# Kernel optimization log

Hardware: AMD Instinct MI355X
Metric: run time of the kernel (lower is better)

Reference implementation:

```python
import jax, jax.numpy as jnp
import numpy as np

N_HEADS = 8
D_K = 64
SCALE = D_K ** -0.5


def setup_inputs() -> dict:
    key = jax.random.key(0)
    ks = jax.random.split(key, 5)
    B, C, H, W = 4, 512, 32, 32
    x = jax.random.normal(ks[0], (B, C, H, W), dtype=jnp.float32)
    Wp = jax.random.normal(ks[1], (3 * N_HEADS * D_K, C), dtype=jnp.float32) * (C ** -0.5)
    bp = jax.random.normal(ks[2], (3 * N_HEADS * D_K,), dtype=jnp.float32) * 0.02
    Wo = jax.random.normal(ks[3], (C, N_HEADS * D_K), dtype=jnp.float32) * ((N_HEADS * D_K) ** -0.5)
    bo = jax.random.normal(ks[4], (C,), dtype=jnp.float32) * 0.02
    return {"x": x, "Wp": Wp, "bp": bp, "Wo": Wo, "bo": bo}


def reference(x, Wp, bp, Wo, bo):
    # x: [B, C, H, W]; NOTE: the torch module defines GroupNorm but never calls it.
    B, C, H, W = x.shape
    s = H * W
    xs = x.reshape(B, C, s).transpose(0, 2, 1)          # [B, s, C]
    qkv = (xs @ Wp.T + bp).reshape(B, s, N_HEADS, 3 * D_K)
    q, k, v = jnp.split(qkv, 3, axis=-1)                 # each [B, s, h, d]
    attn = jnp.einsum('bihd,bjhd->bijh', q, k) * SCALE   # [B, s, s, h]
    attn = jax.nn.softmax(attn, axis=2)                  # softmax over j (keys)
    res = jnp.einsum('bijh,bjhd->bihd', attn, v)         # [B, s, h, d]
    res = res.reshape(B, s, N_HEADS * D_K)
    out = res @ Wo.T + bo + xs                           # residual add
    return out.transpose(0, 2, 1).reshape(B, C, H, W)
```

## Files before the change

kernel.cpp:

```cpp
#include <hip/hip_runtime.h>
#include <hip/hip_bf16.h>

typedef unsigned short u16;
typedef __attribute__((ext_vector_type(8))) short frag_ab;
typedef __attribute__((ext_vector_type(4))) float f32x4;
typedef _Float16 f16;
typedef __attribute__((ext_vector_type(4))) _Float16 f16x4;

#define LOG2E 1.44269504088896f

__device__ __forceinline__ float fast_exp2(float x) {
    return __builtin_amdgcn_exp2f(x);
}

__device__ __forceinline__ void gload_lds16(const u16* g, u16* s) {
    __builtin_amdgcn_global_load_lds((const __attribute__((address_space(1))) void*)g,
                                     (__attribute__((address_space(3))) void*)s, 16, 0, 0);
}

__device__ __forceinline__ void gemm64x128_bt_mainloop(
    const u16* __restrict__ A, const u16* __restrict__ B, int K,
    int m0, int n0, f32x4 acc[2][4], u16* As, u16* Bs)
{
    const int tid = threadIdx.x;
    const int lane = tid & 63, quad = lane >> 4, l16 = lane & 15;
    const int wr = ((tid >> 7) & 1) * 32;
    const int wc = ((tid >> 6) & 1) * 64;
    const int srow = tid >> 3;
    const int scol = (tid & 7) * 8;

    for (int k0 = 0; k0 < K; k0 += 64) {
        __syncthreads();
        #pragma unroll
        for (int p = 0; p < 2; ++p) {
            const int r = srow + p * 32;
            gload_lds16(A + (size_t)(m0 + r) * K + k0 + scol, As + r * 64 + scol);
        }
        #pragma unroll
        for (int p = 0; p < 4; ++p) {
            const int r = srow + p * 32;
            gload_lds16(B + (size_t)(n0 + r) * K + k0 + scol, Bs + r * 64 + scol);
        }
        __syncthreads();
        #pragma unroll
        for (int ks = 0; ks < 2; ++ks) {
            frag_ab a[2], b[4];
            #pragma unroll
            for (int mt = 0; mt < 2; ++mt)
                a[mt] = *(const frag_ab*)(As + (wr + mt * 16 + l16) * 64 + ks * 32 + quad * 8);
            #pragma unroll
            for (int nt = 0; nt < 4; ++nt)
                b[nt] = *(const frag_ab*)(Bs + (wc + nt * 16 + l16) * 64 + ks * 32 + quad * 8);
            #pragma unroll
            for (int mt = 0; mt < 2; ++mt)
                #pragma unroll
                for (int nt = 0; nt < 4; ++nt)
                    acc[mt][nt] = __builtin_amdgcn_mfma_f32_16x16x32_bf16(a[mt], b[nt], acc[mt][nt], 0, 0, 0);
        }
    }
}

__device__ __forceinline__ void gemm64x64_bt_mainloop(
    const u16* __restrict__ A, const u16* __restrict__ B, int K,
    int m0, int n0, f32x4 acc[2][2], u16* As, u16* Bs)
{
    const int tid = threadIdx.x;
    const int lane = tid & 63, quad = lane >> 4, l16 = lane & 15;
    const int wr = ((tid >> 7) & 1) * 32;
    const int wc = ((tid >> 6) & 1) * 32;
    const int srow = tid >> 3;
    const int scol = (tid & 7) * 8;

    for (int k0 = 0; k0 < K; k0 += 64) {
        __syncthreads();
        #pragma unroll
        for (int p = 0; p < 2; ++p) {
            const int r = srow + p * 32;
            gload_lds16(A + (size_t)(m0 + r) * K + k0 + scol, As + r * 64 + scol);
            gload_lds16(B + (size_t)(n0 + r) * K + k0 + scol, Bs + r * 64 + scol);
        }
        __syncthreads();
        #pragma unroll
        for (int ks = 0; ks < 2; ++ks) {
            frag_ab a[2], b[2];
            #pragma unroll
            for (int mt = 0; mt < 2; ++mt)
                a[mt] = *(const frag_ab*)(As + (wr + mt * 16 + l16) * 64 + ks * 32 + quad * 8);
            #pragma unroll
            for (int nt = 0; nt < 2; ++nt)
                b[nt] = *(const frag_ab*)(Bs + (wc + nt * 16 + l16) * 64 + ks * 32 + quad * 8);
            #pragma unroll
            for (int mt = 0; mt < 2; ++mt)
                #pragma unroll
                for (int nt = 0; nt < 2; ++nt)
                    acc[mt][nt] = __builtin_amdgcn_mfma_f32_16x16x32_bf16(a[mt], b[nt], acc[mt][nt], 0, 0, 0);
        }
    }
}

__global__ __launch_bounds__(256) void prep_kernel(
    const float* __restrict__ x, __hip_bfloat16* __restrict__ xs_bf,
    const float* __restrict__ Wp, const float* __restrict__ Wo,
    __hip_bfloat16* __restrict__ w_bf)
{
    __shared__ float tile[32][33];
    const int tid = threadIdx.x;
    const int id = blockIdx.x;
    if (id < 2048) {
        const int i0 = (id & 31) * 32;
        const int c0 = ((id >> 5) & 15) * 32;
        const int b  = id >> 9;
        const int tx = tid & 31, ty = tid >> 5;
        const float* xp = x + ((size_t)b * 512 + c0) * 1024 + i0;
        #pragma unroll
        for (int r = ty; r < 32; r += 8)
            tile[r][tx] = xp[(size_t)r * 1024 + tx];
        __syncthreads();
        __hip_bfloat16* op = xs_bf + ((size_t)b * 1024 + i0) * 512 + c0;
        #pragma unroll
        for (int r = ty; r < 32; r += 8)
            op[(size_t)r * 512 + tx] = __float2bfloat16(tile[tx][r]);
    } else {
        const int t = (id - 2048) * 256 + tid;
        const int i4 = t * 4;
        const float* src = (i4 < 786432) ? (Wp + i4) : (Wo + (i4 - 786432));
        const float4 v = *(const float4*)src;
        ushort4 o;
        o.x = __bfloat16_as_ushort(__float2bfloat16(v.x));
        o.y = __bfloat16_as_ushort(__float2bfloat16(v.y));
        o.z = __bfloat16_as_ushort(__float2bfloat16(v.z));
        o.w = __bfloat16_as_ushort(__float2bfloat16(v.w));
        *(ushort4*)((u16*)w_bf + i4) = o;
    }
}

__global__ __launch_bounds__(256) void qkv_gemm_kernel(
    const u16* __restrict__ Wpb, const u16* __restrict__ xsb,
    const float* __restrict__ bp,
    u16* __restrict__ Qb, u16* __restrict__ Kb, f16* __restrict__ VtT)
{
    __shared__ u16 lds[12288];
    u16* As = lds;
    u16* Bs = lds + 4096;
    f32x4 acc[2][4];
    #pragma unroll
    for (int mt = 0; mt < 2; ++mt)
        #pragma unroll
        for (int nt = 0; nt < 4; ++nt)
            { acc[mt][nt][0]=0.f; acc[mt][nt][1]=0.f; acc[mt][nt][2]=0.f; acc[mt][nt][3]=0.f; }
    const int m0 = blockIdx.y * 64;
    const int n0 = blockIdx.x * 128;
    gemm64x128_bt_mainloop(Wpb, xsb, 512, m0, n0, acc, As, Bs);

    const int tid = threadIdx.x;
    const int lane = tid & 63, quad = lane >> 4, l16 = lane & 15;
    const int wr = ((tid >> 7) & 1) * 32, wc = ((tid >> 6) & 1) * 64;
    const int h = blockIdx.y / 3, part = blockIdx.y % 3;
    const int b = blockIdx.x >> 3, ipb = (blockIdx.x & 7) * 128;
    const size_t bh = (size_t)(b * 8 + h);

    if (part < 2) {
        const float scale = (part == 0) ? (0.125f * LOG2E) : 1.0f;
        __syncthreads();
        u16* T = lds;
        #pragma unroll
        for (int nt = 0; nt < 4; ++nt) {
            const int px = wc + nt * 16 + l16;
            #pragma unroll
            for (int mt = 0; mt < 2; ++mt) {
                const int cb = m0 + wr + mt * 16 + quad * 4;
                ushort4 pk;
                pk.x = __bfloat16_as_ushort(__float2bfloat16((acc[mt][nt][0] + bp[cb + 0]) * scale));
                pk.y = __bfloat16_as_ushort(__float2bfloat16((acc[mt][nt][1] + bp[cb + 1]) * scale));
                pk.z = __bfloat16_as_ushort(__float2bfloat16((acc[mt][nt][2] + bp[cb + 2]) * scale));
                pk.w = __bfloat16_as_ushort(__float2bfloat16((acc[mt][nt][3] + bp[cb + 3]) * scale));
                *(ushort4*)&T[px * 72 + wr + mt * 16 + quad * 4] = pk;
            }
        }
        __syncthreads();
        u16* dst = (part == 0 ? Qb : Kb);
        #pragma unroll
        for (int p = 0; p < 4; ++p) {
            const int row = p * 32 + (tid >> 3);
            const int ch8 = (tid & 7) * 8;
            uint4 rv = *(uint4*)&T[row * 72 + ch8];
            *(uint4*)(dst + ((bh * 1024 + ipb + row) << 6) + ch8) = rv;
        }
    } else {
        f16* dst = VtT + bh * 65536;
        #pragma unroll
        for (int mt = 0; mt < 2; ++mt) {
            #pragma unroll
            for (int r = 0; r < 4; ++r) {
                const int d = wr + mt * 16 + quad * 4 + r;
                const float bias = bp[m0 + d];
                #pragma unroll
                for (int nt = 0; nt < 4; ++nt) {
                    const int j = ipb + wc + nt * 16 + l16;
                    dst[(size_t)(j >> 3) * 512 + d * 8 + (j & 7)] =
                        (f16)(acc[mt][nt][r] + bias);
                }
            }
        }
    }
}

__global__ __launch_bounds__(256, 2) void attn_kernel(
    const u16* __restrict__ Qb, const u16* __restrict__ Kb,
    const f16* __restrict__ VtT, __hip_bfloat16* __restrict__ resb)
{
    __shared__ float Opart[4][32][68];
    __shared__ float Lpart[4][4][16];
    const int bh = blockIdx.x;
    const int it = blockIdx.y;
    const int tid = threadIdx.x;
    const int w = tid >> 6, lane = tid & 63, quad = lane >> 4, l16 = lane & 15;

    const u16* Qp = Qb + (size_t)bh * 65536;
    const u16* Kp = Kb + (size_t)bh * 65536;
    const f16* Vp = VtT + (size_t)bh * 65536;

    frag_ab bq[4][2];
    #pragma unroll
    for (int ig = 0; ig < 4; ++ig) {
        const u16* qptr = Qp + (size_t)(it * 64 + ig * 16 + l16) * 64 + quad * 8;
        bq[ig][0] = *(const frag_ab*)(qptr);
        bq[ig][1] = *(const frag_ab*)(qptr + 32);
    }

    f32x4 o[4][4];
    #pragma unroll
    for (int ig = 0; ig < 4; ++ig)
        #pragma unroll
        for (int dt = 0; dt < 4; ++dt)
            { o[ig][dt][0]=0.f; o[ig][dt][1]=0.f; o[ig][dt][2]=0.f; o[ig][dt][3]=0.f; }
    float l_acc[4] = {0.f, 0.f, 0.f, 0.f};

    const u16* kbase = Kp + (size_t)(w * 32 + l16) * 64 + quad * 8;
    const f16* vbase = Vp + (size_t)(w * 4 + (quad >> 1)) * 512 + l16 * 8 + (quad & 1) * 4;

#define LOADKV(JT, KA, VA) do {                                              \
        const u16* kp_ = kbase + (size_t)(JT) * 8192;                        \
        KA[0][0] = *(const frag_ab*)(kp_);                                   \
        KA[0][1] = *(const frag_ab*)(kp_ + 32);                              \
        KA[1][0] = *(const frag_ab*)(kp_ + 1024);                            \
        KA[1][1] = *(const frag_ab*)(kp_ + 1056);                            \
        const f16* vp_ = vbase + (size_t)(JT) * 8192;                        \
        _Pragma("unroll")                                                    \
        for (int dt_ = 0; dt_ < 4; ++dt_) {                                  \
            VA[dt_][0] = *(const f16x4*)(vp_ + dt_ * 128);                   \
            VA[dt_][1] = *(const f16x4*)(vp_ + 1024 + dt_ * 128);            \
        }                                                                    \
    } while (0)

#define COMPUTE(KA, VA) do {                                                 \
        _Pragma("unroll")                                                    \
        for (int ig = 0; ig < 4; ++ig) {                                     \
            f32x4 st0 = {0.f, 0.f, 0.f, 0.f}, st1 = {0.f, 0.f, 0.f, 0.f};    \
            st0 = __builtin_amdgcn_mfma_f32_16x16x32_bf16(KA[0][0], bq[ig][0], st0, 0, 0, 0); \
            st0 = __builtin_amdgcn_mfma_f32_16x16x32_bf16(KA[0][1], bq[ig][1], st0, 0, 0, 0); \
            st1 = __builtin_amdgcn_mfma_f32_16x16x32_bf16(KA[1][0], bq[ig][0], st1, 0, 0, 0); \
            st1 = __builtin_amdgcn_mfma_f32_16x16x32_bf16(KA[1][1], bq[ig][1], st1, 0, 0, 0); \
            f16x4 p0, p1;                                                    \
            float s = 0.f;                                                   \
            _Pragma("unroll")                                                \
            for (int r = 0; r < 4; ++r) {                                    \
                const float e0 = fast_exp2(st0[r]);                          \
                const float e1 = fast_exp2(st1[r]);                          \
                s += e0 + e1;                                                \
                p0[r] = (f16)e0;                                             \
                p1[r] = (f16)e1;                                             \
            }                                                                \
            l_acc[ig] += s;                                                  \
            _Pragma("unroll")                                                \
            for (int dt = 0; dt < 4; ++dt) {                                 \
                o[ig][dt] = __builtin_amdgcn_mfma_f32_16x16x16f16(VA[dt][0], p0, o[ig][dt], 0, 0, 0); \
                o[ig][dt] = __builtin_amdgcn_mfma_f32_16x16x16f16(VA[dt][1], p1, o[ig][dt], 0, 0, 0); \
            }                                                                \
        }                                                                    \
    } while (0)

    frag_ab ka0[2][2], ka1[2][2];
    f16x4 va0[4][2], va1[4][2];
    LOADKV(0, ka0, va0);
    #pragma unroll
    for (int jt = 0; jt < 8; jt += 2) {
        LOADKV(jt + 1, ka1, va1);
        COMPUTE(ka0, va0);
        if (jt < 6)
            LOADKV(jt + 2, ka0, va0);
        COMPUTE(ka1, va1);
    }
#undef LOADKV
#undef COMPUTE

    #pragma unroll
    for (int ig = 0; ig < 4; ++ig) {
        l_acc[ig] += __shfl_xor(l_acc[ig], 16);
        l_acc[ig] += __shfl_xor(l_acc[ig], 32);
    }
    if (lane < 16) {
        #pragma unroll
        for (int ig = 0; ig < 4; ++ig)
            Lpart[w][ig][lane] = l_acc[ig];
    }

    const int bb = bh >> 3, hh = bh & 7;
    const int il = tid >> 3, d0 = (tid & 7) * 8;
    #pragma unroll
    for (int ph = 0; ph < 2; ++ph) {
        __syncthreads();
        #pragma unroll
        for (int g = 0; g < 2; ++g) {
            const int ig = ph * 2 + g;
            #pragma unroll
            for (int dt = 0; dt < 4; ++dt)
                *(f32x4*)&Opart[w][g * 16 + l16][dt * 16 + quad * 4] = o[ig][dt];
        }
        __syncthreads();
        f32x4 sa = *(const f32x4*)&Opart[0][il][d0];
        f32x4 sb = *(const f32x4*)&Opart[0][il][d0 + 4];
        #pragma unroll
        for (int ww = 1; ww < 4; ++ww) {
            sa += *(const f32x4*)&Opart[ww][il][d0];
            sb += *(const f32x4*)&Opart[ww][il][d0 + 4];
        }
        const int ig = ph * 2 + (il >> 4);
        const float linv = 1.f / (Lpart[0][ig][il & 15] + Lpart[1][ig][il & 15] +
                                  Lpart[2][ig][il & 15] + Lpart[3][ig][il & 15]);
        u16 pk[8];
        #pragma unroll
        for (int e = 0; e < 4; ++e) {
            pk[e]     = __bfloat16_as_ushort(__float2bfloat16(sa[e] * linv));
            pk[e + 4] = __bfloat16_as_ushort(__float2bfloat16(sb[e] * linv));
        }
        u16* orow = (u16*)resb +
            ((size_t)(bb * 1024 + it * 64 + ph * 32 + il)) * 512 + hh * 64 + d0;
        *(uint4*)orow = *(uint4*)pk;
    }
}

__global__ __launch_bounds__(256) void out_gemm_kernel(
    const u16* __restrict__ Wob, const u16* __restrict__ resb,
    const float* __restrict__ bo, const float* __restrict__ x,
    float* __restrict__ out)
{
    __shared__ u16 As[64 * 64];
    __shared__ u16 Bs[64 * 64];
    f32x4 acc[2][2];
    #pragma unroll
    for (int mt = 0; mt < 2; ++mt)
        #pragma unroll
        for (int nt = 0; nt < 2; ++nt)
            { acc[mt][nt][0]=0.f; acc[mt][nt][1]=0.f; acc[mt][nt][2]=0.f; acc[mt][nt][3]=0.f; }
    const int m0 = blockIdx.x * 64;
    const int n0 = blockIdx.y * 64;
    gemm64x64_bt_mainloop(Wob, resb, 512, m0, n0, acc, As, Bs);

    const int tid = threadIdx.x;
    const int lane = tid & 63, quad = lane >> 4, l16 = lane & 15;
    const int wr = ((tid >> 7) & 1) * 32, wc = ((tid >> 6) & 1) * 32;
    #pragma unroll
    for (int nt = 0; nt < 2; ++nt) {
        const int pix = n0 + wc + nt * 16 + l16;
        const int b = pix >> 10, ip = pix & 1023;
        #pragma unroll
        for (int mt = 0; mt < 2; ++mt) {
            #pragma unroll
            for (int r = 0; r < 4; ++r) {
                const int c = m0 + wr + mt * 16 + quad * 4 + r;
                const size_t oidx = (((size_t)b * 512 + c) << 10) + ip;
                out[oidx] = acc[mt][nt][r] + bo[c] + x[oidx];
            }
        }
    }
}

extern "C" void kernel_launch(void* const* d_in, const int* in_sizes, int n_in,
                              void* d_out, int out_size, void* d_ws, size_t ws_size,
                              hipStream_t stream)
{
    const float* x  = (const float*)d_in[0];
    const float* Wp = (const float*)d_in[1];
    const float* bp = (const float*)d_in[2];
    const float* Wo = (const float*)d_in[3];
    const float* bo = (const float*)d_in[4];
    float* out = (float*)d_out;

    char* ws = (char*)d_ws;
    size_t off = 0;
    auto carve = [&](size_t bytes) -> void* {
        void* ptr = ws + off;
        off += (bytes + 255) & ~(size_t)255;
        return ptr;
    };
    __hip_bfloat16* xs_bf = (__hip_bfloat16*)carve((size_t)4096 * 512 * 2);
    __hip_bfloat16* Wp_bf = (__hip_bfloat16*)carve((size_t)1536 * 512 * 2);
    __hip_bfloat16* Wo_bf = (__hip_bfloat16*)carve((size_t)512 * 512 * 2);
    u16*            Qb    = (u16*)carve((size_t)32 * 1024 * 64 * 2);
    u16*            Kb    = (u16*)carve((size_t)32 * 1024 * 64 * 2);
    f16*            VtT   = (f16*)carve((size_t)32 * 1024 * 64 * 2);
    __hip_bfloat16* resb  = (__hip_bfloat16*)carve((size_t)4096 * 512 * 2);

    prep_kernel<<<dim3(3072), 256, 0, stream>>>(x, xs_bf, Wp, Wo, Wp_bf);
    qkv_gemm_kernel<<<dim3(32, 24), 256, 0, stream>>>(
        (const u16*)Wp_bf, (const u16*)xs_bf, bp, Qb, Kb, VtT);
    attn_kernel<<<dim3(32, 16), 256, 0, stream>>>(Qb, Kb, VtT, resb);
    out_gemm_kernel<<<dim3(8, 64), 256, 0, stream>>>(
        (const u16*)Wo_bf, (const u16*)resb, bo, x, out);
    (void)Wo_bf; (void)ws_size; (void)in_sizes; (void)n_in; (void)out_size;
}
```

Measured before the change: 114.5 us.

## Double-buffer LDS tiles in QKV and output GEMM mainloops

Both GEMM mainloops now use two LDS buffers and issue the global-to-LDS loads for the next K tile before computing on the current one, with the K loop fully unrolled for K=512. This overlaps global memory latency with MFMA work and drops one barrier per iteration. In exchange it doubles LDS use per block, which can lower occupancy. The next tile's global_load_lds is also issued without an explicit wait before the closing barrier, so correctness relies on the compiler inserting vmcnt waits. An unused f16 load helper is also added.

Result: faster. 111.0 us (-3.1%).

```diff
diff --git a/kernel.cpp b/kernel.cpp
--- a/kernel.cpp
+++ b/kernel.cpp
@@ -17,10 +17,14 @@
     __builtin_amdgcn_global_load_lds((const __attribute__((address_space(1))) void*)g,
                                      (__attribute__((address_space(3))) void*)s, 16, 0, 0);
 }
+__device__ __forceinline__ void gload_lds16h(const f16* g, f16* s) {
+    __builtin_amdgcn_global_load_lds((const __attribute__((address_space(1))) void*)g,
+                                     (__attribute__((address_space(3))) void*)s, 16, 0, 0);
+}
 
 __device__ __forceinline__ void gemm64x128_bt_mainloop(
-    const u16* __restrict__ A, const u16* __restrict__ B, int K,
-    int m0, int n0, f32x4 acc[2][4], u16* As, u16* Bs)
+    const u16* __restrict__ A, const u16* __restrict__ B,
+    int m0, int n0, f32x4 acc[2][4], u16* lds)
 {
     const int tid = threadIdx.x;
     const int lane = tid & 63, quad = lane >> 4, l16 = lane & 15;
@@ -29,40 +33,56 @@
     const int srow = tid >> 3;
     const int scol = (tid & 7) * 8;
 
-    for (int k0 = 0; k0 < K; k0 += 64) {
-        __syncthreads();
-        #pragma unroll
-        for (int p = 0; p < 2; ++p) {
-            const int r = srow + p * 32;
-            gload_lds16(A + (size_t)(m0 + r) * K + k0 + scol, As + r * 64 + scol);
-        }
-        #pragma unroll
-        for (int p = 0; p < 4; ++p) {
-            const int r = srow + p * 32;
-            gload_lds16(B + (size_t)(n0 + r) * K + k0 + scol, Bs + r * 64 + scol);
-        }
-        __syncthreads();
+    u16* Asb[2] = {lds, lds + 12288};
+    u16* Bsb[2] = {lds + 4096, lds + 16384};
+
+#define STAGE_128(bi, k0) do {                                                \
+        u16* As_ = Asb[bi]; u16* Bs_ = Bsb[bi];                               \
+        _Pragma("unroll")                                                     \
+        for (int p = 0; p < 2; ++p) {                                         \
+            const int r = srow + p * 32;                                      \
+            gload_lds16(A + (size_t)(m0 + r) * 512 + (k0) + scol,             \
+                        As_ + r * 64 + scol);                                 \
+        }                                                                     \
+        _Pragma("unroll")                                                     \
+        for (int p = 0; p < 4; ++p) {                                         \
+            const int r = srow + p * 32;                                      \
+            gload_lds16(B + (size_t)(n0 + r) * 512 + (k0) + scol,             \
+                        Bs_ + r * 64 + scol);                                 \
+        }                                                                     \
+    } while (0)
+
+    STAGE_128(0, 0);
+    __syncthreads();
+    #pragma unroll
+    for (int t = 0; t < 8; ++t) {
+        const int cur = t & 1;
+        if (t < 7) STAGE_128(cur ^ 1, (t + 1) * 64);
+        u16* Asc = Asb[cur];
+        u16* Bsc = Bsb[cur];
         #pragma unroll
         for (int ks = 0; ks < 2; ++ks) {
             frag_ab a[2], b[4];
             #pragma unroll
             for (int mt = 0; mt < 2; ++mt)
-                a[mt] = *(const frag_ab*)(As + (wr + mt * 16 + l16) * 64 + ks * 32 + quad * 8);
+                a[mt] = *(const frag_ab*)(Asc + (wr + mt * 16 + l16) * 64 + ks * 32 + quad * 8);
             #pragma unroll
             for (int nt = 0; nt < 4; ++nt)
-                b[nt] = *(const frag_ab*)(Bs + (wc + nt * 16 + l16) * 64 + ks * 32 + quad * 8);
+                b[nt] = *(const frag_ab*)(Bsc + (wc + nt * 16 + l16) * 64 + ks * 32 + quad * 8);
             #pragma unroll
             for (int mt = 0; mt < 2; ++mt)
                 #pragma unroll
                 for (int nt = 0; nt < 4; ++nt)
                     acc[mt][nt] = __builtin_amdgcn_mfma_f32_16x16x32_bf16(a[mt], b[nt], acc[mt][nt], 0, 0, 0);
         }
-    }
+        if (t < 7) __syncthreads();
+    }
+#undef STAGE_128
 }
 
 __device__ __forceinline__ void gemm64x64_bt_mainloop(
-    const u16* __restrict__ A, const u16* __restrict__ B, int K,
-    int m0, int n0, f32x4 acc[2][2], u16* As, u16* Bs)
+    const u16* __restrict__ A, const u16* __restrict__ B,
+    int m0, int n0, f32x4 acc[2][2], u16* lds)
 {
     const int tid = threadIdx.x;
     const int lane = tid & 63, quad = lane >> 4, l16 = lane & 15;
@@ -71,31 +91,47 @@
     const int srow = tid >> 3;
     const int scol = (tid & 7) * 8;
 
-    for (int k0 = 0; k0 < K; k0 += 64) {
-        __syncthreads();
-        #pragma unroll
-        for (int p = 0; p < 2; ++p) {
-            const int r = srow + p * 32;
-            gload_lds16(A + (size_t)(m0 + r) * K + k0 + scol, As + r * 64 + scol);
-            gload_lds16(B + (size_t)(n0 + r) * K + k0 + scol, Bs + r * 64 + scol);
-        }
-        __syncthreads();
+    u16* Asb[2] = {lds, lds + 8192};
+    u16* Bsb[2] = {lds + 4096, lds + 12288};
+
+#define STAGE_64(bi, k0) do {                                                 \
+        u16* As_ = Asb[bi]; u16* Bs_ = Bsb[bi];                               \
+        _Pragma("unroll")                                                     \
+        for (int p = 0; p < 2; ++p) {                                         \
+            const int r = srow + p * 32;                                      \
+            gload_lds16(A + (size_t)(m0 + r) * 512 + (k0) + scol,             \
+                        As_ + r * 64 + scol);                                 \
+            gload_lds16(B + (size_t)(n0 + r) * 512 + (k0) + scol,             \
+                        Bs_ + r * 64 + scol);                                 \
+        }                                                                     \
+    } while (0)
+
+    STAGE_64(0, 0);
+    __syncthreads();
+    #pragma unroll
+    for (int t = 0; t < 8; ++t) {
+        const int cur = t & 1;
+        if (t < 7) STAGE_64(cur ^ 1, (t + 1) * 64);
+        u16* Asc = Asb[cur];
+        u16* Bsc = Bsb[cur];
         #pragma unroll
         for (int ks = 0; ks < 2; ++ks) {
             frag_ab a[2], b[2];
             #pragma unroll
             for (int mt = 0; mt < 2; ++mt)
-                a[mt] = *(const frag_ab*)(As + (wr + mt * 16 + l16) * 64 + ks * 32 + quad * 8);
+                a[mt] = *(const frag_ab*)(Asc + (wr + mt * 16 + l16) * 64 + ks * 32 + quad * 8);
             #pragma unroll
             for (int nt = 0; nt < 2; ++nt)
-                b[nt] = *(const frag_ab*)(Bs + (wc + nt * 16 + l16) * 64 + ks * 32 + quad * 8);
+                b[nt] = *(const frag_ab*)(Bsc + (wc + nt * 16 + l16) * 64 + ks * 32 + quad * 8);
             #pragma unroll
             for (int mt = 0; mt < 2; ++mt)
                 #pragma unroll
                 for (int nt = 0; nt < 2; ++nt)
                     acc[mt][nt] = __builtin_amdgcn_mfma_f32_16x16x32_bf16(a[mt], b[nt], acc[mt][nt], 0, 0, 0);
         }
-    }
+        if (t < 7) __syncthreads();
+    }
+#undef STAGE_64
 }
 
 __global__ __launch_bounds__(256) void prep_kernel(
@@ -139,9 +175,7 @@
     const float* __restrict__ bp,
     u16* __restrict__ Qb, u16* __restrict__ Kb, f16* __restrict__ VtT)
 {
-    __shared__ u16 lds[12288];
-    u16* As = lds;
-    u16* Bs = lds + 4096;
+    __shared__ u16 lds[24576];
     f32x4 acc[2][4];
     #pragma unroll
     for (int mt = 0; mt < 2; ++mt)
@@ -150,7 +184,7 @@
             { acc[mt][nt][0]=0.f; acc[mt][nt][1]=0.f; acc[mt][nt][2]=0.f; acc[mt][nt][3]=0.f; }
     const int m0 = blockIdx.y * 64;
     const int n0 = blockIdx.x * 128;
-    gemm64x128_bt_mainloop(Wpb, xsb, 512, m0, n0, acc, As, Bs);
+    gemm64x128_bt_mainloop(Wpb, xsb, m0, n0, acc, lds);
 
     const int tid = threadIdx.x;
     const int lane = tid & 63, quad = lane >> 4, l16 = lane & 15;
@@ -345,8 +379,7 @@
     const float* __restrict__ bo, const float* __restrict__ x,
     float* __restrict__ out)
 {
-    __shared__ u16 As[64 * 64];
-    __shared__ u16 Bs[64 * 64];
+    __shared__ u16 lds[16384];
     f32x4 acc[2][2];
     #pragma unroll
     for (int mt = 0; mt < 2; ++mt)
@@ -355,7 +388,7 @@
             { acc[mt][nt][0]=0.f; acc[mt][nt][1]=0.f; acc[mt][nt][2]=0.f; acc[mt][nt][3]=0.f; }
     const int m0 = blockIdx.x * 64;
     const int n0 = blockIdx.y * 64;
-    gemm64x64_bt_mainloop(Wob, resb, 512, m0, n0, acc, As, Bs);
+    gemm64x64_bt_mainloop(Wob, resb, m0, n0, acc, lds);
 
     const int tid = threadIdx.x;
     const int lane = tid & 63, quad = lane >> 4, l16 = lane & 15;
```
